# Kernel tuning notes

Hardware: AMD Instinct MI355X
Metric: run time of the kernel (lower is better)

The kernel has to match this reference:

```python
import jax, jax.numpy as jnp
import numpy as np

N = 50000   # nodes
E = 800000  # edges
H = 128     # hidden dim
V = 50000   # feats_per_node (embedding vocab)


def setup_inputs() -> dict:
    key = jax.random.key(0)
    ks = jax.random.split(key, 16)
    s = 0.05  # keep activations in a sane range
    return {
        "node_ids": jax.random.randint(ks[0], (N,), 0, V),
        "src": jax.random.randint(ks[1], (E,), 0, N),
        "dst": jnp.sort(jax.random.randint(ks[2], (E,), 0, N)),
        "emb": jax.random.normal(ks[3], (V, H), jnp.float32) * s,
        "W_pool1": jax.random.normal(ks[4], (H, H), jnp.float32) * s,
        "b_pool1": jax.random.normal(ks[5], (H,), jnp.float32) * s,
        "W_self1": jax.random.normal(ks[6], (H, H), jnp.float32) * s,
        "W_neigh1": jax.random.normal(ks[7], (H, H), jnp.float32) * s,
        "b1": jax.random.normal(ks[8], (H,), jnp.float32) * s,
        "W_pool2": jax.random.normal(ks[9], (H, H), jnp.float32) * s,
        "b_pool2": jax.random.normal(ks[10], (H,), jnp.float32) * s,
        "W_self2": jax.random.normal(ks[11], (H, H), jnp.float32) * s,
        "W_neigh2": jax.random.normal(ks[12], (H, H), jnp.float32) * s,
        "b2": jax.random.normal(ks[13], (H,), jnp.float32) * s,
    }


def _sage_pool_layer(h, src, dst, W_pool, b_pool, W_self, W_neigh, b):
    # DGL SAGEConv('pool'): per-src MLP, gather over edges, segmented max per dst.
    m = jax.nn.relu(h @ W_pool + b_pool)              # [N, H]
    msgs = m[src]                                     # [E, H] gather
    agg = jax.ops.segment_max(msgs, dst, num_segments=N,
                              indices_are_sorted=True)  # [N, H]
    agg = jnp.where(jnp.isneginf(agg), 0.0, agg)      # zero-in-degree -> 0 (DGL semantics)
    return h @ W_self + agg @ W_neigh + b


def reference(node_ids, src, dst, emb,
              W_pool1, b_pool1, W_self1, W_neigh1, b1,
              W_pool2, b_pool2, W_self2, W_neigh2, b2):
    h = emb[node_ids]                                 # embedding_h on 1-hot indices
    h = _sage_pool_layer(h, src, dst, W_pool1, b_pool1, W_self1, W_neigh1, b1)
    h = _sage_pool_layer(h, src, dst, W_pool2, b_pool2, W_self2, W_neigh2, b2)
    return h
```

## Files before the change

kernel.cpp:

```cpp
#include <hip/hip_runtime.h>

#define HD 128

typedef __attribute__((ext_vector_type(8))) short short8;
typedef __attribute__((ext_vector_type(4))) float floatx4;
typedef __attribute__((ext_vector_type(2))) unsigned short ushort2v;
typedef __attribute__((ext_vector_type(4))) unsigned int uint4v;

typedef unsigned short ushort_t;
typedef unsigned int uint_t;

__device__ __forceinline__ ushort_t f2b(float f) {
    union { float f; uint_t u; } v; v.f = f;
    uint_t r = v.u + 0x7fff + ((v.u >> 16) & 1);
    return (ushort_t)(r >> 16);
}
__device__ __forceinline__ short8 cvt8(const float* __restrict__ p) {
    float4 u = *(const float4*)p, v = *(const float4*)(p + 4);
    short8 r;
    r[0] = (short)f2b(u.x); r[1] = (short)f2b(u.y); r[2] = (short)f2b(u.z); r[3] = (short)f2b(u.w);
    r[4] = (short)f2b(v.x); r[5] = (short)f2b(v.y); r[6] = (short)f2b(v.z); r[7] = (short)f2b(v.w);
    return r;
}
__device__ __forceinline__ uint_t pkmax(uint_t a, uint_t b) {
    return __builtin_bit_cast(uint_t,
        __builtin_elementwise_max(__builtin_bit_cast(ushort2v, a),
                                  __builtin_bit_cast(ushort2v, b)));
}
__device__ __forceinline__ int lbound(const int* __restrict__ dst, int E, int v) {
    int lo = 0, hi = E;
    while (lo < hi) {
        int mid = (lo + hi) >> 1;
        if (dst[mid] < v) lo = mid + 1; else hi = mid;
    }
    return lo;
}

__global__ __launch_bounds__(256) void k_prep(const int* __restrict__ dst, int E,
                                              const int* __restrict__ src,
                                              int* __restrict__ rp, int N,
                                              int* __restrict__ srcPad,
                                              const float* W0, const float* W1,
                                              const float* W2, const float* W3,
                                              const float* W4, const float* W5,
                                              ushort_t* __restrict__ Wpk,
                                              int nbR, int nbP) {
    int b = blockIdx.x;
    if (b < nbR) {
        int i = b * 256 + threadIdx.x;
        if (i > N) return;
        rp[i] = lbound(dst, E, i);
    } else if (b < nbR + nbP) {
        int bb = b - nbR;
        const float* Ws[6] = {W0, W1, W2, W3, W4, W5};
        int mat = bb >> 6;
        int o = ((bb & 63) << 8) + threadIdx.x;
        int j = o & 7, l = (o >> 3) & 63, s = (o >> 9) & 3, t = o >> 11;
        int k = s * 32 + ((l >> 4) & 3) * 8 + j;
        int n = t * 16 + (l & 15);
        Wpk[(size_t)mat * 16384 + o] = f2b(Ws[mat][k * HD + n]);
    } else {
        int idx = (b - nbR - nbP) * 256 + threadIdx.x;
        int node = idx >> 5;
        if (node >= N) return;
        int j = idx & 31;
        int lane = threadIdx.x & 63;
        int half = (lane & 31) >> 4;
        int lo = lbound(dst, E, node + half);
        int base = lane & 32;
        int beg = __shfl(lo, base);
        int end = __shfl(lo, base + 16);
        int deg = end - beg;
        int val = 0;
        if (deg > 0) val = src[beg + (j < deg ? j : deg - 1)];
        srcPad[(size_t)node * 32 + j] = val;
    }
}

__device__ __forceinline__ void stage_w(const ushort_t* __restrict__ g,
                                        ushort_t* l, int tid) {
#pragma unroll
    for (int i = 0; i < 8; ++i) {
        int off = i * 2048 + tid * 8;
        *(short8*)&l[off] = *(const short8*)&g[off];
    }
}
__device__ __forceinline__ void stage_w_half(const ushort_t* __restrict__ g,
                                             ushort_t* l, int tid) {
#pragma unroll
    for (int i = 0; i < 4; ++i) {
        int off = i * 2048 + tid * 8;
        *(short8*)&l[off] = *(const short8*)&g[off];
    }
}

__device__ __forceinline__ void store_bf16(ushort_t* __restrict__ m, int row,
                                           int colbase, const floatx4& acc,
                                           const float4& bv, bool relu, int N) {
    if (row >= N) return;
    float v0 = acc[0] + bv.x, v1 = acc[1] + bv.y, v2 = acc[2] + bv.z, v3 = acc[3] + bv.w;
    if (relu) { v0 = fmaxf(v0, 0.f); v1 = fmaxf(v1, 0.f); v2 = fmaxf(v2, 0.f); v3 = fmaxf(v3, 0.f); }
    uint2 o; o.x = (uint_t)f2b(v0) | ((uint_t)f2b(v1) << 16);
    o.y = (uint_t)f2b(v2) | ((uint_t)f2b(v3) << 16);
    *(uint2*)&m[(size_t)row * HD + colbase] = o;
}

__device__ __forceinline__ void store_m(ushort_t* __restrict__ m, int row,
                                        int colbase, const floatx4& acc,
                                        const float4& bv, int N) {
    if (row >= N) return;
    float v0 = fmaxf(acc[0] + bv.x, 0.f), v1 = fmaxf(acc[1] + bv.y, 0.f);
    float v2 = fmaxf(acc[2] + bv.z, 0.f), v3 = fmaxf(acc[3] + bv.w, 0.f);
    uint2 o; o.x = (uint_t)f2b(v0) | ((uint_t)f2b(v1) << 16);
    o.y = (uint_t)f2b(v2) | ((uint_t)f2b(v3) << 16);
    size_t addr = (size_t)(colbase >> 5) * ((size_t)N * 32)
                + (size_t)row * 32 + (colbase & 31);
    *(uint2*)&m[addr] = o;
}

__global__ __launch_bounds__(256) void k_gather_pool(const int* __restrict__ ids,
                                                     const float* __restrict__ emb,
                                                     const ushort_t* __restrict__ Wpk,
                                                     const float* __restrict__ bias,
                                                     ushort_t* __restrict__ h0,
                                                     ushort_t* __restrict__ m, int N) {
    __shared__ ushort_t Wl[16384];
    int wave = blockIdx.x * 4 + (threadIdx.x >> 6);
    int row0 = wave * 32;
    int l = threadIdx.x & 63;
    int ar0 = row0 + (l & 15); if (ar0 >= N) ar0 = N - 1;
    int ar1 = ar0 + 16;        if (ar1 >= N) ar1 = N - 1;
    int ac = (l >> 4) * 8;
    int id0 = ids[ar0], id1 = ids[ar1];
    short8 a0[4], a1[4];
#pragma unroll
    for (int s = 0; s < 4; ++s) {
        a0[s] = cvt8(&emb[(size_t)id0 * HD + s * 32 + ac]);
        a1[s] = cvt8(&emb[(size_t)id1 * HD + s * 32 + ac]);
    }
    stage_w(Wpk, Wl, threadIdx.x);
    __syncthreads();
    if (row0 >= N) return;
#pragma unroll
    for (int s = 0; s < 4; ++s) {
        *(short8*)&h0[(size_t)ar0 * HD + s * 32 + ac] = a0[s];
        *(short8*)&h0[(size_t)ar1 * HD + s * 32 + ac] = a1[s];
    }
    int g0 = row0 + (l & 15), g1 = g0 + 16;
    int cb0 = ((l >> 4) & 3) * 4;
#pragma unroll
    for (int t = 0; t < 8; ++t) {
        floatx4 acc0 = {0.f, 0.f, 0.f, 0.f};
        floatx4 acc1 = {0.f, 0.f, 0.f, 0.f};
#pragma unroll
        for (int s = 0; s < 4; ++s) {
            short8 w = *(const short8*)&Wl[(t * 4 + s) * 512 + l * 8];
            acc0 = __builtin_amdgcn_mfma_f32_16x16x32_bf16(w, a0[s], acc0, 0, 0, 0);
            acc1 = __builtin_amdgcn_mfma_f32_16x16x32_bf16(w, a1[s], acc1, 0, 0, 0);
        }
        int cb = t * 16 + cb0;
        float4 bv = *(const float4*)&bias[cb];
        store_m(m, g0, cb, acc0, bv, N);
        store_m(m, g1, cb, acc1, bv, N);
    }
}

__global__ __launch_bounds__(256) void k_pool(const ushort_t* __restrict__ h,
                                              const ushort_t* __restrict__ Wpk,
                                              const float* __restrict__ bias,
                                              ushort_t* __restrict__ m, int N) {
    __shared__ ushort_t Wl[8192];
    int colhalf = blockIdx.x & 1;
    int wave = (blockIdx.x >> 1) * 4 + (threadIdx.x >> 6);
    int row0 = wave * 32;
    int l = threadIdx.x & 63;
    int ar0 = row0 + (l & 15); if (ar0 >= N) ar0 = N - 1;
    int ar1 = ar0 + 16;        if (ar1 >= N) ar1 = N - 1;
    int ac = (l >> 4) * 8;
    short8 a0[4], a1[4];
#pragma unroll
    for (int s = 0; s < 4; ++s) {
        a0[s] = *(const short8*)&h[(size_t)ar0 * HD + s * 32 + ac];
        a1[s] = *(const short8*)&h[(size_t)ar1 * HD + s * 32 + ac];
    }
    stage_w_half(Wpk + colhalf * 8192, Wl, threadIdx.x);
    __syncthreads();
    if (row0 >= N) return;
    int g0 = row0 + (l & 15), g1 = g0 + 16;
    int cb0 = ((l >> 4) & 3) * 4;
#pragma unroll
    for (int t = 0; t < 4; ++t) {
        floatx4 acc0 = {0.f, 0.f, 0.f, 0.f};
        floatx4 acc1 = {0.f, 0.f, 0.f, 0.f};
#pragma unroll
        for (int s = 0; s < 4; ++s) {
            short8 w = *(const short8*)&Wl[(t * 4 + s) * 512 + l * 8];
            acc0 = __builtin_amdgcn_mfma_f32_16x16x32_bf16(w, a0[s], acc0, 0, 0, 0);
            acc1 = __builtin_amdgcn_mfma_f32_16x16x32_bf16(w, a1[s], acc1, 0, 0, 0);
        }
        int cb = (colhalf * 4 + t) * 16 + cb0;
        float4 bv = *(const float4*)&bias[cb];
        store_m(m, g0, cb, acc0, bv, N);
        store_m(m, g1, cb, acc1, bv, N);
    }
}

__global__ __launch_bounds__(256) void k_segmax(const ushort_t* __restrict__ m,
                                                const int* __restrict__ srcPad,
                                                const int* __restrict__ src,
                                                const int* __restrict__ rp,
                                                ushort_t* __restrict__ agg, int N) {
    int cg = blockIdx.x & 3;
    int l = threadIdx.x & 63;
    int slot = l >> 2;
    int c = l & 3;
    int node0 = ((blockIdx.x >> 2) * 4 + (threadIdx.x >> 6)) * 4;
    if (node0 >= N) return;
    const uint_t* __restrict__ mg = (const uint_t*)m + (size_t)cg * ((size_t)N * 16);
    uint_t* __restrict__ aggw = (uint_t*)agg;

    int nd[4], s0[4], s1[4], deg[4];
#pragma unroll
    for (int nn = 0; nn < 4; ++nn) {
        int node = node0 + nn; if (node >= N) node = N - 1;
        nd[nn] = node;
    }
#pragma unroll
    for (int nn = 0; nn < 4; ++nn) {
        s0[nn] = srcPad[(size_t)nd[nn] * 32 + slot];
        s1[nn] = srcPad[(size_t)nd[nn] * 32 + 16 + slot];
    }
#pragma unroll
    for (int nn = 0; nn < 4; ++nn)
        deg[nn] = rp[nd[nn] + 1] - rp[nd[nn]];
    uint4v p0[4], p1[4];
#pragma unroll
    for (int nn = 0; nn < 4; ++nn) {
        p0[nn] = *(const uint4v*)&mg[(size_t)s0[nn] * 16 + c * 4];
        p1[nn] = *(const uint4v*)&mg[(size_t)s1[nn] * 16 + c * 4];
    }
    int b0 = slot & 1, b1 = (slot >> 1) & 1;
#pragma unroll
    for (int nn = 0; nn < 4; ++nn) {
        int node = node0 + nn;
        if (node >= N) continue;
        uint_t a0 = 0u, a1 = 0u, a2 = 0u, a3 = 0u;
        if (deg[nn] > 0) {
            a0 = pkmax(p0[nn].x, p1[nn].x);
            a1 = pkmax(p0[nn].y, p1[nn].y);
            a2 = pkmax(p0[nn].z, p1[nn].z);
            a3 = pkmax(p0[nn].w, p1[nn].w);
        }
        if (deg[nn] > 32) {
            int beg = rp[node];
            int dm1 = deg[nn] - 1;
            for (int o = 32; o < deg[nn]; o += 16) {
                int i = o + slot; if (i > dm1) i = dm1;
                int s = src[beg + i];
                uint4v p = *(const uint4v*)&mg[(size_t)s * 16 + c * 4];
                a0 = pkmax(a0, p.x); a1 = pkmax(a1, p.y);
                a2 = pkmax(a2, p.z); a3 = pkmax(a3, p.w);
            }
        }
        uint_t q0 = b0 ? a2 : a0, q1 = b0 ? a3 : a1;
        uint_t r0 = b0 ? a0 : a2, r1 = b0 ? a1 : a3;
        q0 = pkmax(q0, (uint_t)__shfl_xor((int)r0, 4));
        q1 = pkmax(q1, (uint_t)__shfl_xor((int)r1, 4));
        uint_t s_ = b1 ? q1 : q0, t_ = b1 ? q0 : q1;
        s_ = pkmax(s_, (uint_t)__shfl_xor((int)t_, 8));
        s_ = pkmax(s_, (uint_t)__shfl_xor((int)s_, 16));
        s_ = pkmax(s_, (uint_t)__shfl_xor((int)s_, 32));
        if (slot < 4)
            __builtin_nontemporal_store(s_,
                &aggw[(size_t)node * 64 + cg * 16 + c * 4 + 2 * b0 + b1]);
    }
}

template <bool F32OUT>
__global__ __launch_bounds__(256) void k_dual(const ushort_t* __restrict__ h,
                                              const ushort_t* __restrict__ agg,
                                              const ushort_t* __restrict__ WsPk,
                                              const ushort_t* __restrict__ WnPk,
                                              const float* __restrict__ bias,
                                              void* __restrict__ outp, int N) {
    __shared__ ushort_t Wl[16384];
    int colhalf = blockIdx.x & 1;
    int wave = (blockIdx.x >> 1) * 4 + (threadIdx.x >> 6);
    int row0 = wave * 32;
    int l = threadIdx.x & 63;
    int ar0 = row0 + (l & 15); if (ar0 >= N) ar0 = N - 1;
    int ar1 = ar0 + 16;        if (ar1 >= N) ar1 = N - 1;
    int ac = (l >> 4) * 8;
    short8 ah0[4], ah1[4], ag0[4], ag1[4];
#pragma unroll
    for (int s = 0; s < 4; ++s) {
        ah0[s] = *(const short8*)&h[(size_t)ar0 * HD + s * 32 + ac];
        ah1[s] = *(const short8*)&h[(size_t)ar1 * HD + s * 32 + ac];
        ag0[s] = *(const short8*)&agg[(size_t)ar0 * HD + s * 32 + ac];
        ag1[s] = *(const short8*)&agg[(size_t)ar1 * HD + s * 32 + ac];
    }
    stage_w_half(WsPk + colhalf * 8192, Wl, threadIdx.x);
    stage_w_half(WnPk + colhalf * 8192, Wl + 8192, threadIdx.x);
    __syncthreads();
    if (row0 >= N) return;
    int g0 = row0 + (l & 15), g1 = g0 + 16;
    int cb0 = ((l >> 4) & 3) * 4;
#pragma unroll
    for (int t = 0; t < 4; ++t) {
        floatx4 acc0 = {0.f, 0.f, 0.f, 0.f};
        floatx4 acc1 = {0.f, 0.f, 0.f, 0.f};
#pragma unroll
        for (int s = 0; s < 4; ++s) {
            short8 ws = *(const short8*)&Wl[(t * 4 + s) * 512 + l * 8];
            acc0 = __builtin_amdgcn_mfma_f32_16x16x32_bf16(ws, ah0[s], acc0, 0, 0, 0);
            acc1 = __builtin_amdgcn_mfma_f32_16x16x32_bf16(ws, ah1[s], acc1, 0, 0, 0);
        }
#pragma unroll
        for (int s = 0; s < 4; ++s) {
            short8 wn = *(const short8*)&Wl[8192 + (t * 4 + s) * 512 + l * 8];
            acc0 = __builtin_amdgcn_mfma_f32_16x16x32_bf16(wn, ag0[s], acc0, 0, 0, 0);
            acc1 = __builtin_amdgcn_mfma_f32_16x16x32_bf16(wn, ag1[s], acc1, 0, 0, 0);
        }
        int cb = (colhalf * 4 + t) * 16 + cb0;
        float4 bv = *(const float4*)&bias[cb];
        if (F32OUT) {
            float* out = (float*)outp;
            if (g0 < N) {
                float4 v = make_float4(acc0[0] + bv.x, acc0[1] + bv.y,
                                       acc0[2] + bv.z, acc0[3] + bv.w);
                *(float4*)&out[(size_t)g0 * HD + cb] = v;
            }
            if (g1 < N) {
                float4 v = make_float4(acc1[0] + bv.x, acc1[1] + bv.y,
                                       acc1[2] + bv.z, acc1[3] + bv.w);
                *(float4*)&out[(size_t)g1 * HD + cb] = v;
            }
        } else {
            ushort_t* out = (ushort_t*)outp;
            store_bf16(out, g0, cb, acc0, bv, false, N);
            store_bf16(out, g1, cb, acc1, bv, false, N);
        }
    }
}

extern "C" void kernel_launch(void* const* d_in, const int* in_sizes, int n_in,
                              void* d_out, int out_size, void* d_ws, size_t ws_size,
                              hipStream_t stream) {
    const int*   node_ids = (const int*)d_in[0];
    const int*   src      = (const int*)d_in[1];
    const int*   dst      = (const int*)d_in[2];
    const float* emb      = (const float*)d_in[3];
    const float* Wp1      = (const float*)d_in[4];
    const float* bp1      = (const float*)d_in[5];
    const float* Ws1      = (const float*)d_in[6];
    const float* Wn1      = (const float*)d_in[7];
    const float* b1       = (const float*)d_in[8];
    const float* Wp2      = (const float*)d_in[9];
    const float* bp2      = (const float*)d_in[10];
    const float* Ws2      = (const float*)d_in[11];
    const float* Wn2      = (const float*)d_in[12];
    const float* b2       = (const float*)d_in[13];
    float* out = (float*)d_out;

    const int N = in_sizes[0];
    const int E = in_sizes[1];

    char* ws = (char*)d_ws;
    int* rp = (int*)ws;
    size_t off = (((size_t)(N + 1) * 4) + 255) & ~(size_t)255;
    int* srcPad = (int*)(ws + off);
    off += (((size_t)N * 32 * 4) + 255) & ~(size_t)255;
    ushort_t* Wpk  = (ushort_t*)(ws + off);
    ushort_t* h0   = Wpk + 6 * 16384;
    ushort_t* h1   = h0 + (size_t)N * HD;
    ushort_t* bufM = h1 + (size_t)N * HD;
    ushort_t* bufA = bufM + (size_t)N * HD;

    const int nbR = (N + 1 + 255) / 256;
    const int nbP = 6 * 64;
    const int nbS = ((N * 32) + 255) / 256;
    const int nb_gemm = (N + 127) / 128;
    const int nb_half = nb_gemm * 2;
    const int nb_seg  = ((N + 15) / 16) * 4;

    k_prep<<<nbR + nbP + nbS, 256, 0, stream>>>(dst, E, src, rp, N, srcPad,
                                                Wp1, Ws1, Wn1, Wp2, Ws2, Wn2,
                                                Wpk, nbR, nbP);

    const ushort_t* Wp1k = Wpk;
    const ushort_t* Ws1k = Wpk + 16384;
    const ushort_t* Wn1k = Wpk + 2 * 16384;
    const ushort_t* Wp2k = Wpk + 3 * 16384;
    const ushort_t* Ws2k = Wpk + 4 * 16384;
    const ushort_t* Wn2k = Wpk + 5 * 16384;

    k_gather_pool<<<nb_gemm, 256, 0, stream>>>(node_ids, emb, Wp1k, bp1, h0, bufM, N);
    k_segmax<<<nb_seg, 256, 0, stream>>>(bufM, srcPad, src, rp, bufA, N);
    k_dual<false><<<nb_half, 256, 0, stream>>>(h0, bufA, Ws1k, Wn1k, b1, h1, N);
    k_pool<<<nb_half, 256, 0, stream>>>(h1, Wp2k, bp2, bufM, N);
    k_segmax<<<nb_seg, 256, 0, stream>>>(bufM, srcPad, src, rp, bufA, N);
    k_dual<true><<<nb_half, 256, 0, stream>>>(h1, bufA, Ws2k, Wn2k, b2, out, N);
}
```

Before: 246.4 us.

## Build padded neighbor table via edge scatter with sentinel zero row

Replaces the per-node binary-search construction of the padded source table with a sentinel fill in the prep kernel and an edge-parallel scatter fused into the first gather/pool launch. Padding slots now point to an extra zero row appended to the message buffer, which removes the degree checks and per-node branches in the segmented max. The intent is to cut the per-node lower-bound searches and the divergent branching. The cost is an extra row in the message layout, and the scatter adds reads of dst and rp per edge. Using zero as the identity relies on the messages being non-negative after the ReLU.

```diff
diff --git a/kernel.cpp b/kernel.cpp
--- a/kernel.cpp
+++ b/kernel.cpp
@@ -37,9 +37,9 @@
 }
 
 __global__ __launch_bounds__(256) void k_prep(const int* __restrict__ dst, int E,
-                                              const int* __restrict__ src,
                                               int* __restrict__ rp, int N,
                                               int* __restrict__ srcPad,
+                                              ushort_t* __restrict__ bufM,
                                               const float* W0, const float* W1,
                                               const float* W2, const float* W3,
                                               const float* W4, const float* W5,
@@ -60,20 +60,14 @@
         int n = t * 16 + (l & 15);
         Wpk[(size_t)mat * 16384 + o] = f2b(Ws[mat][k * HD + n]);
     } else {
-        int idx = (b - nbR - nbP) * 256 + threadIdx.x;
-        int node = idx >> 5;
-        if (node >= N) return;
-        int j = idx & 31;
-        int lane = threadIdx.x & 63;
-        int half = (lane & 31) >> 4;
-        int lo = lbound(dst, E, node + half);
-        int base = lane & 32;
-        int beg = __shfl(lo, base);
-        int end = __shfl(lo, base + 16);
-        int deg = end - beg;
-        int val = 0;
-        if (deg > 0) val = src[beg + (j < deg ? j : deg - 1)];
-        srcPad[(size_t)node * 32 + j] = val;
+        int bb = b - nbR - nbP;
+        if (bb == 0 && threadIdx.x < 64) {
+            uint_t* mz = (uint_t*)bufM;
+            mz[(size_t)(threadIdx.x >> 4) * ((size_t)(N + 1) * 16)
+               + (size_t)N * 16 + (threadIdx.x & 15)] = 0u;
+        }
+        int idx = bb * 256 + threadIdx.x;
+        if (idx < N * 32) srcPad[idx] = N;
     }
 }
 
@@ -113,7 +107,7 @@
     float v2 = fmaxf(acc[2] + bv.z, 0.f), v3 = fmaxf(acc[3] + bv.w, 0.f);
     uint2 o; o.x = (uint_t)f2b(v0) | ((uint_t)f2b(v1) << 16);
     o.y = (uint_t)f2b(v2) | ((uint_t)f2b(v3) << 16);
-    size_t addr = (size_t)(colbase >> 5) * ((size_t)N * 32)
+    size_t addr = (size_t)(colbase >> 5) * ((size_t)(N + 1) * 32)
                 + (size_t)row * 32 + (colbase & 31);
     *(uint2*)&m[addr] = o;
 }
@@ -123,7 +117,21 @@
                                                      const ushort_t* __restrict__ Wpk,
                                                      const float* __restrict__ bias,
                                                      ushort_t* __restrict__ h0,
-                                                     ushort_t* __restrict__ m, int N) {
+                                                     ushort_t* __restrict__ m, int N,
+                                                     const int* __restrict__ src,
+                                                     const int* __restrict__ dst,
+                                                     const int* __restrict__ rp,
+                                                     int* __restrict__ srcPad,
+                                                     int E, int nb_gemm) {
+    if ((int)blockIdx.x >= nb_gemm) {
+        int e = (blockIdx.x - nb_gemm) * 256 + threadIdx.x;
+        if (e < E) {
+            int node = dst[e];
+            int j = e - rp[node];
+            if (j < 32) srcPad[(size_t)node * 32 + j] = src[e];
+        }
+        return;
+    }
     __shared__ ushort_t Wl[16384];
     int wave = blockIdx.x * 4 + (threadIdx.x >> 6);
     int row0 = wave * 32;
@@ -216,10 +224,10 @@
     int c = l & 3;
     int node0 = ((blockIdx.x >> 2) * 4 + (threadIdx.x >> 6)) * 4;
     if (node0 >= N) return;
-    const uint_t* __restrict__ mg = (const uint_t*)m + (size_t)cg * ((size_t)N * 16);
+    const uint_t* __restrict__ mg = (const uint_t*)m + (size_t)cg * ((size_t)(N + 1) * 16);
     uint_t* __restrict__ aggw = (uint_t*)agg;
 
-    int nd[4], s0[4], s1[4], deg[4];
+    int nd[4], s0[4], s1[4], bg[4], en[4];
 #pragma unroll
     for (int nn = 0; nn < 4; ++nn) {
         int node = node0 + nn; if (node >= N) node = N - 1;
@@ -231,8 +239,10 @@
         s1[nn] = srcPad[(size_t)nd[nn] * 32 + 16 + slot];
     }
 #pragma unroll
-    for (int nn = 0; nn < 4; ++nn)
-        deg[nn] = rp[nd[nn] + 1] - rp[nd[nn]];
+    for (int nn = 0; nn < 4; ++nn) {
+        bg[nn] = rp[nd[nn]];
+        en[nn] = rp[nd[nn] + 1];
+    }
     uint4v p0[4], p1[4];
 #pragma unroll
     for (int nn = 0; nn < 4; ++nn) {
@@ -243,20 +253,16 @@
 #pragma unroll
     for (int nn = 0; nn < 4; ++nn) {
         int node = node0 + nn;
-        if (node >= N) continue;
-        uint_t a0 = 0u, a1 = 0u, a2 = 0u, a3 = 0u;
-        if (deg[nn] > 0) {
-            a0 = pkmax(p0[nn].x, p1[nn].x);
-            a1 = pkmax(p0[nn].y, p1[nn].y);
-            a2 = pkmax(p0[nn].z, p1[nn].z);
-            a3 = pkmax(p0[nn].w, p1[nn].w);
-        }
-        if (deg[nn] > 32) {
-            int beg = rp[node];
-            int dm1 = deg[nn] - 1;
-            for (int o = 32; o < deg[nn]; o += 16) {
+        uint_t a0 = pkmax(p0[nn].x, p1[nn].x);
+        uint_t a1 = pkmax(p0[nn].y, p1[nn].y);
+        uint_t a2 = pkmax(p0[nn].z, p1[nn].z);
+        uint_t a3 = pkmax(p0[nn].w, p1[nn].w);
+        int deg = en[nn] - bg[nn];
+        if (__builtin_expect(deg > 32, 0)) {
+            int dm1 = deg - 1;
+            for (int o = 32; o < deg; o += 16) {
                 int i = o + slot; if (i > dm1) i = dm1;
-                int s = src[beg + i];
+                int s = src[bg[nn] + i];
                 uint4v p = *(const uint4v*)&mg[(size_t)s * 16 + c * 4];
                 a0 = pkmax(a0, p.x); a1 = pkmax(a1, p.y);
                 a2 = pkmax(a2, p.z); a3 = pkmax(a3, p.w);
@@ -270,7 +276,7 @@
         s_ = pkmax(s_, (uint_t)__shfl_xor((int)t_, 8));
         s_ = pkmax(s_, (uint_t)__shfl_xor((int)s_, 16));
         s_ = pkmax(s_, (uint_t)__shfl_xor((int)s_, 32));
-        if (slot < 4)
+        if (slot < 4 && node < N)
             __builtin_nontemporal_store(s_,
                 &aggw[(size_t)node * 64 + cg * 16 + c * 4 + 2 * b0 + b1]);
     }
@@ -374,16 +380,17 @@
     ushort_t* h0   = Wpk + 6 * 16384;
     ushort_t* h1   = h0 + (size_t)N * HD;
     ushort_t* bufM = h1 + (size_t)N * HD;
-    ushort_t* bufA = bufM + (size_t)N * HD;
+    ushort_t* bufA = bufM + (size_t)(N + 1) * HD;
 
     const int nbR = (N + 1 + 255) / 256;
     const int nbP = 6 * 64;
-    const int nbS = ((N * 32) + 255) / 256;
+    const int nbI = ((N * 32) + 255) / 256;
+    const int nbE = (E + 255) / 256;
     const int nb_gemm = (N + 127) / 128;
     const int nb_half = nb_gemm * 2;
     const int nb_seg  = ((N + 15) / 16) * 4;
 
-    k_prep<<<nbR + nbP + nbS, 256, 0, stream>>>(dst, E, src, rp, N, srcPad,
+    k_prep<<<nbR + nbP + nbI, 256, 0, stream>>>(dst, E, rp, N, srcPad, bufM,
                                                 Wp1, Ws1, Wn1, Wp2, Ws2, Wn2,
                                                 Wpk, nbR, nbP);
 
@@ -394,7 +401,9 @@
     const ushort_t* Ws2k = Wpk + 4 * 16384;
     const ushort_t* Wn2k = Wpk + 5 * 16384;
 
-    k_gather_pool<<<nb_gemm, 256, 0, stream>>>(node_ids, emb, Wp1k, bp1, h0, bufM, N);
+    k_gather_pool<<<nb_gemm + nbE, 256, 0, stream>>>(node_ids, emb, Wp1k, bp1,
+                                                     h0, bufM, N,
+                                                     src, dst, rp, srcPad, E, nb_gemm);
     k_segmax<<<nb_seg, 256, 0, stream>>>(bufM, srcPad, src, rp, bufA, N);
     k_dual<false><<<nb_half, 256, 0, stream>>>(h0, bufA, Ws1k, Wn1k, b1, h1, N);
     k_pool<<<nb_half, 256, 0, stream>>>(h1, Wp2k, bp2, bufM, N);
```

New measurement: 228.3 us. -7.3%, faster.
